# Performance work log

Measured on AMD Instinct MI355X. Metric: run time of the kernel, lower is better.

Reference implementation:

```python
import jax, jax.numpy as jnp
import numpy as np

H = 32; W = 32; C = 128; K = 3
FS = K * K                      # filter_size = 9
CH = H - K + 1; CW = W - K + 1
F = CH * CW                     # num_convs = 900
HW = H * W                      # 1024
TEMP = 1.0                      # softmax_temp
EPS = 1e-5                      # masked_softmax epsilon
B = 8


def _build_masks():
    # local_indices[f] = flat indices of the K x K window f (row-major),
    # matching compute_input_mask with stride=1, no stochastic stride.
    idx = np.zeros((F, FS), dtype=np.int32)
    f = 0
    for i in range(CH):
        for j in range(CW):
            rows = np.arange(i, i + K)[:, None]
            cols = np.arange(j, j + K)[None, :]
            idx[f] = (rows * W + cols).reshape(-1)
            f += 1
    # global mask = (1 - local_mask) * (1 - padding_mask); padding_mask == 0 for 'valid'
    gmask = np.ones((F, HW), dtype=np.float32)
    gmask[np.arange(F)[:, None], idx] = 0.0
    return jnp.asarray(idx), jnp.asarray(gmask)


def setup_inputs() -> dict:
    key = jax.random.key(0)
    ks = jax.random.split(key, 8)
    bound = 1.0 / np.sqrt(C)  # torch nn.Linear default init
    u = lambda k, shape: jax.random.uniform(k, shape, jnp.float32, -bound, bound)
    batch = jax.random.normal(ks[0], (B, H, W, C), jnp.float32)
    Wq = u(ks[1], (C, C)); bq = u(ks[2], (C,))
    Wk = u(ks[3], (C, C)); bk = u(ks[4], (C,))
    wv = u(ks[5], (C, 1)); bv = u(ks[6], (1,))
    local_indices, gmask = _build_masks()
    return {"batch": batch, "Wq": Wq, "bq": bq, "Wk": Wk, "bk": bk,
            "wv": wv, "bv": bv, "gmask": gmask, "local_indices": local_indices}


def reference(batch, Wq, bq, Wk, bk, wv, bv, gmask, local_indices):
    # Approach '4': per-window local queries attend over global (non-window)
    # pixels; scalar values gate the local patch pixels; gated patch sums to
    # one output pixel per window. Valid padding => local pixels are unmasked
    # and the masked softmax zeroes out window/padding positions, so the
    # per-window masked linear transforms reduce exactly to full-image
    # transforms gathered/masked afterwards (no [F,B,H,W,C] materialization).
    b = batch.shape[0]
    xf = batch.reshape(b, HW, C)
    Q = xf @ Wq.T + bq                         # [B,HW,C] query_transform
    Kf = xf @ Wk.T + bk                        # [B,HW,C] key_transform
    V = (xf @ wv + bv)[..., 0]                 # [B,HW]   value_transform (C->1)
    Qg = Q[:, local_indices]                   # [B,F,FS,C] local queries (gather)
    Xl = xf[:, local_indices]                  # [B,F,FS,C] local patch features
    compat = jnp.einsum('bfpc,bqc->bfpq', Qg, Kf) / TEMP   # [B,F,FS,HW]
    # masked_softmax: exp * mask / (sum + eps), no max-subtraction (faithful)
    exps = jnp.exp(compat) * gmask[None, :, None, :]
    attn = exps / (exps.sum(-1, keepdims=True) + EPS)
    gates = jnp.einsum('bfpq,bq->bfp', attn, V)            # [B,F,FS] scalar gates
    out = jnp.einsum('bfp,bfpc->bfc', gates, Xl)           # [B,F,C]
    return out.reshape(b, CH, CW, C)
```

## Files before the change

### kernel.cpp

```cpp
#include <hip/hip_runtime.h>

#define BATCH 8
#define HW_N  1024
#define CD    128
#define W_IMG 32
#define CH_O  30
#define F_N   900

#define OFF_Q16 0u
#define OFF_K16 2097152u
#define OFF_V   4194304u
#define OFF_D   4227072u
#define OFF_TP  5046272u
#define OFF_TVP 5570560u
#define OFF_WQF 6094848u
#define OFF_WKF 6127616u

typedef _Float16 f16x8 __attribute__((ext_vector_type(8)));
typedef _Float16 f16x4 __attribute__((ext_vector_type(4)));
typedef float    f32x4 __attribute__((ext_vector_type(4)));

__device__ __forceinline__ size_t frag_off(int R, int k) {
    return (size_t)(R >> 4) * 2048 +
           (size_t)((((k >> 5) * 4 + ((k >> 3) & 3)) * 128) + ((R & 15) * 8) + (k & 7));
}

__device__ __forceinline__ void async16(const void* g, void* l) {
    __builtin_amdgcn_global_load_lds(
        (const __attribute__((address_space(1))) unsigned int*)g,
        (__attribute__((address_space(3))) unsigned int*)l,
        16, 0, 0);
}

__global__ __launch_bounds__(256) void prep_kernel(
    const float* __restrict__ Wq, const float* __restrict__ Wk,
    _Float16* __restrict__ WqF, _Float16* __restrict__ WkF)
{
    int id = blockIdx.x * 256 + threadIdx.x;
    int c  = id >> 4;
    int kc = id & 15;
    size_t src = (size_t)c * CD + kc * 8;
    size_t dst = frag_off(c, kc * 8);

    float vq[8], vk[8];
    *(float4*)&vq[0] = *(const float4*)&Wq[src];
    *(float4*)&vq[4] = *(const float4*)&Wq[src + 4];
    *(float4*)&vk[0] = *(const float4*)&Wk[src];
    *(float4*)&vk[4] = *(const float4*)&Wk[src + 4];

    f16x8 qh, kh;
#pragma unroll
    for (int e = 0; e < 8; ++e) {
        qh[e] = (_Float16)vq[e];
        kh[e] = (_Float16)vk[e];
    }
    *(f16x8*)&WqF[dst] = qh;
    *(f16x8*)&WkF[dst] = kh;
}

__global__ __launch_bounds__(256) void qkv_kernel(
    const float* __restrict__ xf,
    const float* __restrict__ bq, const float* __restrict__ bk,
    const float* __restrict__ wv, const float* __restrict__ bv,
    const _Float16* __restrict__ WqF, const _Float16* __restrict__ WkF,
    _Float16* __restrict__ Q16, _Float16* __restrict__ K16,
    float* __restrict__ V)
{
    __shared__ float    xs[16][132];
    __shared__ _Float16 xh[2048];

    const int t = threadIdx.x;
    const int rowbase = blockIdx.x * 16;

#pragma unroll
    for (int m = 0; m < 2; ++m) {
        int id = t + 256 * m;
        int r  = id >> 5;
        int c4 = id & 31;
        float4 v4 = *(const float4*)&xf[(size_t)(rowbase + r) * CD + c4 * 4];
        *(float4*)&xs[r][c4 * 4] = v4;
        int c = c4 * 4;
        int off = ((c >> 5) * 4 + ((c >> 3) & 3)) * 128 + r * 8 + (c & 7);
        f16x4 hh;
        hh[0] = (_Float16)v4.x; hh[1] = (_Float16)v4.y;
        hh[2] = (_Float16)v4.z; hh[3] = (_Float16)v4.w;
        *(f16x4*)&xh[off] = hh;
    }
    __syncthreads();

    const int w    = t >> 6;
    const int lane = t & 63;
    const int q    = lane >> 4;
    const int i    = lane & 15;

    f32x4 aq[2], ak[2];
#pragma unroll
    for (int ct = 0; ct < 2; ++ct) {
        aq[ct] = (f32x4){0.f, 0.f, 0.f, 0.f};
        ak[ct] = (f32x4){0.f, 0.f, 0.f, 0.f};
    }

#pragma unroll
    for (int ks = 0; ks < 4; ++ks) {
        const int aoff = (ks * 4 + q) * 128 + i * 8;
        f16x8 ah = *(f16x8*)&xh[aoff];
#pragma unroll
        for (int ct = 0; ct < 2; ++ct) {
            size_t boff = (size_t)(w * 2 + ct) * 2048 + (size_t)(ks * 4 + q) * 128 + i * 8;
            f16x8 bq8 = *(const f16x8*)&WqF[boff];
            f16x8 bk8 = *(const f16x8*)&WkF[boff];
            aq[ct] = __builtin_amdgcn_mfma_f32_16x16x32_f16(ah, bq8, aq[ct], 0, 0, 0);
            ak[ct] = __builtin_amdgcn_mfma_f32_16x16x32_f16(ah, bk8, ak[ct], 0, 0, 0);
        }
    }

#pragma unroll
    for (int ct = 0; ct < 2; ++ct) {
        int c = (w * 2 + ct) * 16 + i;
        float bqv = bq[c], bkv = bk[c];
#pragma unroll
        for (int g = 0; g < 4; ++g) {
            int R = rowbase + q * 4 + g;
            size_t o = frag_off(R, c);
            Q16[o] = (_Float16)(aq[ct][g] + bqv);
            K16[o] = (_Float16)(ak[ct][g] + bkv);
        }
    }

    if (t < 16) {
        float s = 0.f;
#pragma unroll 8
        for (int k = 0; k < CD; ++k) s += xs[t][k] * wv[k];
        V[rowbase + t] = s + bv[0];
    }
}

#define A_OFF 0
#define B_OFF 16384
#define VS_OFF 32768
#define SCR2 16896
#define ATTN_LDS_TOTAL 33792

__global__ __launch_bounds__(256) void attn_kernel(
    const _Float16* __restrict__ Q16, const _Float16* __restrict__ K16,
    const float* __restrict__ V,
    double* __restrict__ Tp, double* __restrict__ TVp,
    float* __restrict__ D)
{
    extern __shared__ char lds[];
    _Float16* Ah = (_Float16*)(lds + A_OFF);
    _Float16* Bh = (_Float16*)(lds + B_OFF);
    float*    Vs = (float*)(lds + VS_OFF);

    const int b  = blockIdx.x;
    const int rb = blockIdx.y;
    const int cb = blockIdx.z;
    const int t  = threadIdx.x;
    const int w    = t >> 6;
    const int lane = t & 63;
    const int q    = lane >> 4;
    const int i    = lane & 15;
    const int wy = w >> 1, wx = w & 1;

    if (t < 128) Vs[t] = V[b * HW_N + cb * 128 + t];

    f32x4 acc[4][4];
#pragma unroll
    for (int r = 0; r < 4; ++r)
#pragma unroll
        for (int f = 0; f < 4; ++f) acc[r][f] = (f32x4){0.f, 0.f, 0.f, 0.f};

    const size_t abase = (size_t)(b * 8 + rb) * 16384;
    const size_t bbase = (size_t)(b * 8 + cb) * 16384;

    for (int kh = 0; kh < 2; ++kh) {
        __syncthreads();
#pragma unroll
        for (int m = 0; m < 4; ++m) {
            int id = t + 256 * m;
            size_t goff = (size_t)(id >> 7) * 2048 + kh * 1024 + (id & 127) * 8;
            int loff = id * 8;
            async16(Q16 + abase + goff, Ah + loff);
            async16(K16 + bbase + goff, Bh + loff);
        }
        asm volatile("s_waitcnt vmcnt(0)" ::: "memory");
        __syncthreads();

#pragma unroll
        for (int kcl = 0; kcl < 2; ++kcl) {
            f16x8 a4[4], b4[4];
#pragma unroll
            for (int r = 0; r < 4; ++r) {
                int ao = (((wy * 4 + r) * 2 + kcl) * 4 + q) * 128 + i * 8;
                a4[r] = *(f16x8*)&Ah[ao];
                int bo = (((wx * 4 + r) * 2 + kcl) * 4 + q) * 128 + i * 8;
                b4[r] = *(f16x8*)&Bh[bo];
            }
#pragma unroll
            for (int r = 0; r < 4; ++r)
#pragma unroll
                for (int f = 0; f < 4; ++f)
                    acc[r][f] = __builtin_amdgcn_mfma_f32_16x16x32_f16(
                        a4[r], b4[f], acc[r][f], 0, 0, 0);
        }
    }

    float st[4][4], stv[4][4];
#pragma unroll
    for (int r = 0; r < 4; ++r)
#pragma unroll
        for (int g = 0; g < 4; ++g) { st[r][g] = 0.f; stv[r][g] = 0.f; }

    const bool band = (cb - rb <= 1) && (rb - cb <= 1);

#pragma unroll
    for (int f = 0; f < 4; ++f) {
        int col_local = wx * 64 + f * 16 + i;
        int hw_c = cb * 128 + col_local;
        float v = Vs[col_local];
        int cimg_r = hw_c >> 5, cimg_c = hw_c & 31;
#pragma unroll
        for (int r = 0; r < 4; ++r)
#pragma unroll
            for (int g = 0; g < 4; ++g) {
                float e = __expf(acc[r][f][g]);
                st[r][g]  += e;
                stv[r][g] += e * v;
                if (band) {
                    int row_local = wy * 64 + r * 16 + q * 4 + g;
                    int hw_r = rb * 128 + row_local;
                    int dy = cimg_r - (hw_r >> 5);
                    int dx = cimg_c - (hw_r & 31);
                    if ((unsigned)(dy + 2) <= 4u && (unsigned)(dx + 2) <= 4u)
                        D[(size_t)(b * HW_N + hw_r) * 25 + (dy + 2) * 5 + (dx + 2)] = e;
                }
            }
    }

    __syncthreads();
    float* scrT  = (float*)lds;
    float* scrTV = (float*)(lds + SCR2);
#pragma unroll
    for (int r = 0; r < 4; ++r)
#pragma unroll
        for (int g = 0; g < 4; ++g) {
            int rl = wy * 64 + r * 16 + q * 4 + g;
            scrT [rl * 33 + wx * 16 + i] = st[r][g];
            scrTV[rl * 33 + wx * 16 + i] = stv[r][g];
        }
    __syncthreads();
    if (t < 128) {
        double s = 0.0;
#pragma unroll
        for (int c = 0; c < 32; ++c) s += (double)scrT[t * 33 + c];
        Tp[(size_t)(b * HW_N + rb * 128 + t) * 8 + cb] = s;
    } else {
        int tt = t - 128;
        double s = 0.0;
#pragma unroll
        for (int c = 0; c < 32; ++c) s += (double)scrTV[tt * 33 + c];
        TVp[(size_t)(b * HW_N + rb * 128 + tt) * 8 + cb] = s;
    }
}

__global__ __launch_bounds__(256) void gate_out_kernel(
    const float* __restrict__ xf, const float* __restrict__ V,
    const double* __restrict__ Tp, const double* __restrict__ TVp,
    const float* __restrict__ D, float* __restrict__ out)
{
    const int fi = blockIdx.x;
    const int b  = blockIdx.y;
    const int t  = threadIdx.x;

    __shared__ float  xs[96 * 128];
    __shared__ float  gates[32][9];
    __shared__ double Ts[96], TVs[96];

#pragma unroll
    for (int m = 0; m < 12; ++m) {
        int id   = t + 256 * m;
        int srow = id >> 5;
        int c4   = id & 31;
        int r3   = srow >> 5, colc = srow & 31;
        *(float4*)&xs[srow * 128 + c4 * 4] =
            *(const float4*)&xf[((size_t)(b * 32 + fi + r3) * 32 + colc) * CD + c4 * 4];
    }

    if (t < 96) {
        int R = b * HW_N + (fi + (t >> 5)) * W_IMG + (t & 31);
        double s = 0.0;
#pragma unroll
        for (int c = 0; c < 8; ++c) s += Tp[(size_t)R * 8 + c];
        Ts[t] = s;
    } else if (t >= 128 && t < 224) {
        int tt = t - 128;
        int R = b * HW_N + (fi + (tt >> 5)) * W_IMG + (tt & 31);
        double s = 0.0;
#pragma unroll
        for (int c = 0; c < 8; ++c) s += TVp[(size_t)R * 8 + c];
        TVs[tt] = s;
    }
    __syncthreads();

    for (int g = t; g < 270; g += 256) {
        int fj = g / 9, p = g % 9;
        int pr = p / 3, pc = p % 3;
        int lrow = pr * 32 + fj + pc;
        int ip = (fi + pr) * W_IMG + (fj + pc);
        const float* Drow = &D[(size_t)(b * HW_N + ip) * 25];
        double se = 0.0, sev = 0.0;
#pragma unroll
        for (int qq = 0; qq < 9; ++qq) {
            int qr = qq / 3, qc = qq % 3;
            float e = Drow[(qr - pr + 2) * 5 + (qc - pc + 2)];
            se  += (double)e;
            sev += (double)(e * V[b * HW_N + (fi + qr) * W_IMG + (fj + qc)]);
        }
        double denom = Ts[lrow] - se + 1e-5;
        double numer = TVs[lrow] - sev;
        gates[fj][p] = (float)(numer / denom);
    }
    __syncthreads();

    const int c4  = t & 31;
    const int fjl = t >> 5;
#pragma unroll
    for (int it = 0; it < 4; ++it) {
        int fj = fjl + 8 * it;
        if (fj < CH_O) {
            f32x4 o = (f32x4){0.f, 0.f, 0.f, 0.f};
#pragma unroll
            for (int p = 0; p < 9; ++p) {
                int pr = p / 3, pc = p % 3;
                f32x4 x = *(f32x4*)&xs[(pr * 32 + fj + pc) * 128 + c4 * 4];
                float gv = gates[fj][p];
                o += gv * x;
            }
            *(f32x4*)&out[((size_t)(b * F_N) + fi * CH_O + fj) * CD + c4 * 4] = o;
        }
    }
}

extern "C" void kernel_launch(void* const* d_in, const int* in_sizes, int n_in,
                              void* d_out, int out_size, void* d_ws, size_t ws_size,
                              hipStream_t stream)
{
    (void)in_sizes; (void)n_in; (void)out_size; (void)ws_size;
    const float* batch = (const float*)d_in[0];
    const float* Wq    = (const float*)d_in[1];
    const float* bq    = (const float*)d_in[2];
    const float* Wk    = (const float*)d_in[3];
    const float* bk    = (const float*)d_in[4];
    const float* wv    = (const float*)d_in[5];
    const float* bv    = (const float*)d_in[6];

    char*      ws  = (char*)d_ws;
    _Float16*  Q16 = (_Float16*)(ws + OFF_Q16);
    _Float16*  K16 = (_Float16*)(ws + OFF_K16);
    float*     V   = (float*)(ws + OFF_V);
    float*     D   = (float*)(ws + OFF_D);
    double*    Tp  = (double*)(ws + OFF_TP);
    double*    TVp = (double*)(ws + OFF_TVP);
    _Float16*  WqF = (_Float16*)(ws + OFF_WQF);
    _Float16*  WkF = (_Float16*)(ws + OFF_WKF);
    float*     out = (float*)d_out;

    prep_kernel<<<dim3(8), dim3(256), 0, stream>>>(Wq, Wk, WqF, WkF);
    qkv_kernel<<<dim3(512), dim3(256), 0, stream>>>(batch, bq, bk, wv, bv,
                                                    WqF, WkF, Q16, K16, V);
    attn_kernel<<<dim3(8, 8, 8), dim3(256), ATTN_LDS_TOTAL, stream>>>(
        Q16, K16, V, Tp, TVp, D);
    gate_out_kernel<<<dim3(CH_O, BATCH), dim3(256), 0, stream>>>(batch, V, Tp, TVp, D, out);
}
```

Baseline: 96.78 us.

## Fuse weight conversion into QKV, stage outputs via LDS, single-shot attn load, split gate kernel

Drops the separate weight-prep kernel: each QKV block now loads fp32 Wq/Wk from global and converts them to fp16 fragments in registers. Q/K tiles are staged through LDS so the global stores become coalesced 16-byte writes, and the V dot product is spread over 128 threads with a shuffle reduction. The attention kernel loads the full K=128 Q and K tiles into 64KB of LDS in one pass instead of two halves, which removes a barrier round but raises LDS use per block and may lower occupancy. The gate/output kernel is split over two channel halves to double the grid and halve its LDS footprint, at the cost of recomputing the gates in both halves.

```diff
diff --git a/kernel.cpp b/kernel.cpp
--- a/kernel.cpp
+++ b/kernel.cpp
@@ -13,17 +13,10 @@
 #define OFF_D   4227072u
 #define OFF_TP  5046272u
 #define OFF_TVP 5570560u
-#define OFF_WQF 6094848u
-#define OFF_WKF 6127616u
 
 typedef _Float16 f16x8 __attribute__((ext_vector_type(8)));
 typedef _Float16 f16x4 __attribute__((ext_vector_type(4)));
 typedef float    f32x4 __attribute__((ext_vector_type(4)));
-
-__device__ __forceinline__ size_t frag_off(int R, int k) {
-    return (size_t)(R >> 4) * 2048 +
-           (size_t)((((k >> 5) * 4 + ((k >> 3) & 3)) * 128) + ((R & 15) * 8) + (k & 7));
-}
 
 __device__ __forceinline__ void async16(const void* g, void* l) {
     __builtin_amdgcn_global_load_lds(
@@ -32,45 +25,47 @@
         16, 0, 0);
 }
 
-__global__ __launch_bounds__(256) void prep_kernel(
-    const float* __restrict__ Wq, const float* __restrict__ Wk,
-    _Float16* __restrict__ WqF, _Float16* __restrict__ WkF)
-{
-    int id = blockIdx.x * 256 + threadIdx.x;
-    int c  = id >> 4;
-    int kc = id & 15;
-    size_t src = (size_t)c * CD + kc * 8;
-    size_t dst = frag_off(c, kc * 8);
-
-    float vq[8], vk[8];
-    *(float4*)&vq[0] = *(const float4*)&Wq[src];
-    *(float4*)&vq[4] = *(const float4*)&Wq[src + 4];
-    *(float4*)&vk[0] = *(const float4*)&Wk[src];
-    *(float4*)&vk[4] = *(const float4*)&Wk[src + 4];
-
-    f16x8 qh, kh;
-#pragma unroll
-    for (int e = 0; e < 8; ++e) {
-        qh[e] = (_Float16)vq[e];
-        kh[e] = (_Float16)vk[e];
-    }
-    *(f16x8*)&WqF[dst] = qh;
-    *(f16x8*)&WkF[dst] = kh;
+__device__ __forceinline__ f16x8 cvt8(const float* __restrict__ p) {
+    float4 a = *(const float4*)p;
+    float4 b = *(const float4*)(p + 4);
+    f16x8 h;
+    h[0] = (_Float16)a.x; h[1] = (_Float16)a.y;
+    h[2] = (_Float16)a.z; h[3] = (_Float16)a.w;
+    h[4] = (_Float16)b.x; h[5] = (_Float16)b.y;
+    h[6] = (_Float16)b.z; h[7] = (_Float16)b.w;
+    return h;
 }
 
 __global__ __launch_bounds__(256) void qkv_kernel(
     const float* __restrict__ xf,
+    const float* __restrict__ Wq, const float* __restrict__ Wk,
     const float* __restrict__ bq, const float* __restrict__ bk,
     const float* __restrict__ wv, const float* __restrict__ bv,
-    const _Float16* __restrict__ WqF, const _Float16* __restrict__ WkF,
     _Float16* __restrict__ Q16, _Float16* __restrict__ K16,
     float* __restrict__ V)
 {
     __shared__ float    xs[16][132];
     __shared__ _Float16 xh[2048];
+    __shared__ _Float16 qtile[2048];
+    __shared__ _Float16 ktile[2048];
 
     const int t = threadIdx.x;
     const int rowbase = blockIdx.x * 16;
+    const int w    = t >> 6;
+    const int lane = t & 63;
+    const int q    = lane >> 4;
+    const int i    = lane & 15;
+
+    f16x8 wqf[2][4], wkf[2][4];
+#pragma unroll
+    for (int ct = 0; ct < 2; ++ct) {
+        const size_t c = (size_t)((w * 2 + ct) * 16 + i);
+#pragma unroll
+        for (int ks = 0; ks < 4; ++ks) {
+            wqf[ct][ks] = cvt8(&Wq[c * CD + ks * 32 + q * 8]);
+            wkf[ct][ks] = cvt8(&Wk[c * CD + ks * 32 + q * 8]);
+        }
+    }
 
 #pragma unroll
     for (int m = 0; m < 2; ++m) {
@@ -88,11 +83,6 @@
     }
     __syncthreads();
 
-    const int w    = t >> 6;
-    const int lane = t & 63;
-    const int q    = lane >> 4;
-    const int i    = lane & 15;
-
     f32x4 aq[2], ak[2];
 #pragma unroll
     for (int ct = 0; ct < 2; ++ct) {
@@ -106,11 +96,8 @@
         f16x8 ah = *(f16x8*)&xh[aoff];
 #pragma unroll
         for (int ct = 0; ct < 2; ++ct) {
-            size_t boff = (size_t)(w * 2 + ct) * 2048 + (size_t)(ks * 4 + q) * 128 + i * 8;
-            f16x8 bq8 = *(const f16x8*)&WqF[boff];
-            f16x8 bk8 = *(const f16x8*)&WkF[boff];
-            aq[ct] = __builtin_amdgcn_mfma_f32_16x16x32_f16(ah, bq8, aq[ct], 0, 0, 0);
-            ak[ct] = __builtin_amdgcn_mfma_f32_16x16x32_f16(ah, bk8, ak[ct], 0, 0, 0);
+            aq[ct] = __builtin_amdgcn_mfma_f32_16x16x32_f16(ah, wqf[ct][ks], aq[ct], 0, 0, 0);
+            ak[ct] = __builtin_amdgcn_mfma_f32_16x16x32_f16(ah, wkf[ct][ks], ak[ct], 0, 0, 0);
         }
     }
 
@@ -118,28 +105,42 @@
     for (int ct = 0; ct < 2; ++ct) {
         int c = (w * 2 + ct) * 16 + i;
         float bqv = bq[c], bkv = bk[c];
+        int coff = ((c >> 5) * 4 + ((c >> 3) & 3)) * 128 + (c & 7);
 #pragma unroll
         for (int g = 0; g < 4; ++g) {
-            int R = rowbase + q * 4 + g;
-            size_t o = frag_off(R, c);
-            Q16[o] = (_Float16)(aq[ct][g] + bqv);
-            K16[o] = (_Float16)(ak[ct][g] + bkv);
-        }
-    }
-
-    if (t < 16) {
+            int off = coff + (q * 4 + g) * 8;
+            qtile[off] = (_Float16)(aq[ct][g] + bqv);
+            ktile[off] = (_Float16)(ak[ct][g] + bkv);
+        }
+    }
+    __syncthreads();
+
+    {
+        f16x8 qv = *(f16x8*)&qtile[t * 8];
+        f16x8 kv = *(f16x8*)&ktile[t * 8];
+        *(f16x8*)&Q16[(size_t)rowbase * 128 + t * 8] = qv;
+        *(f16x8*)&K16[(size_t)rowbase * 128 + t * 8] = kv;
+    }
+
+    if (t < 128) {
+        int r = t >> 3, l = t & 7;
         float s = 0.f;
-#pragma unroll 8
-        for (int k = 0; k < CD; ++k) s += xs[t][k] * wv[k];
-        V[rowbase + t] = s + bv[0];
+#pragma unroll
+        for (int k = 0; k < 16; ++k) {
+            int c = l + k * 8;
+            s += xs[r][c] * wv[c];
+        }
+        s += __shfl_xor(s, 1);
+        s += __shfl_xor(s, 2);
+        s += __shfl_xor(s, 4);
+        if (l == 0) V[rowbase + r] = s + bv[0];
     }
 }
 
 #define A_OFF 0
-#define B_OFF 16384
-#define VS_OFF 32768
+#define B_OFF 32768
 #define SCR2 16896
-#define ATTN_LDS_TOTAL 33792
+#define ATTN_LDS_TOTAL 65536
 
 __global__ __launch_bounds__(256) void attn_kernel(
     const _Float16* __restrict__ Q16, const _Float16* __restrict__ K16,
@@ -150,7 +151,7 @@
     extern __shared__ char lds[];
     _Float16* Ah = (_Float16*)(lds + A_OFF);
     _Float16* Bh = (_Float16*)(lds + B_OFF);
-    float*    Vs = (float*)(lds + VS_OFF);
+    __shared__ float Vs[128];
 
     const int b  = blockIdx.x;
     const int rb = blockIdx.y;
@@ -164,45 +165,40 @@
 
     if (t < 128) Vs[t] = V[b * HW_N + cb * 128 + t];
 
-    f32x4 acc[4][4];
-#pragma unroll
-    for (int r = 0; r < 4; ++r)
-#pragma unroll
-        for (int f = 0; f < 4; ++f) acc[r][f] = (f32x4){0.f, 0.f, 0.f, 0.f};
-
     const size_t abase = (size_t)(b * 8 + rb) * 16384;
     const size_t bbase = (size_t)(b * 8 + cb) * 16384;
 
-    for (int kh = 0; kh < 2; ++kh) {
-        __syncthreads();
-#pragma unroll
-        for (int m = 0; m < 4; ++m) {
-            int id = t + 256 * m;
-            size_t goff = (size_t)(id >> 7) * 2048 + kh * 1024 + (id & 127) * 8;
-            int loff = id * 8;
-            async16(Q16 + abase + goff, Ah + loff);
-            async16(K16 + bbase + goff, Bh + loff);
-        }
-        asm volatile("s_waitcnt vmcnt(0)" ::: "memory");
-        __syncthreads();
-
-#pragma unroll
-        for (int kcl = 0; kcl < 2; ++kcl) {
-            f16x8 a4[4], b4[4];
-#pragma unroll
-            for (int r = 0; r < 4; ++r) {
-                int ao = (((wy * 4 + r) * 2 + kcl) * 4 + q) * 128 + i * 8;
-                a4[r] = *(f16x8*)&Ah[ao];
-                int bo = (((wx * 4 + r) * 2 + kcl) * 4 + q) * 128 + i * 8;
-                b4[r] = *(f16x8*)&Bh[bo];
-            }
-#pragma unroll
-            for (int r = 0; r < 4; ++r)
-#pragma unroll
-                for (int f = 0; f < 4; ++f)
-                    acc[r][f] = __builtin_amdgcn_mfma_f32_16x16x32_f16(
-                        a4[r], b4[f], acc[r][f], 0, 0, 0);
-        }
+#pragma unroll
+    for (int m = 0; m < 8; ++m) {
+        int id = t + 256 * m;
+        async16(Q16 + abase + (size_t)id * 8, Ah + id * 8);
+        async16(K16 + bbase + (size_t)id * 8, Bh + id * 8);
+    }
+    asm volatile("s_waitcnt vmcnt(0)" ::: "memory");
+    __syncthreads();
+
+    f32x4 acc[4][4];
+#pragma unroll
+    for (int r = 0; r < 4; ++r)
+#pragma unroll
+        for (int f = 0; f < 4; ++f) acc[r][f] = (f32x4){0.f, 0.f, 0.f, 0.f};
+
+#pragma unroll
+    for (int kcl = 0; kcl < 4; ++kcl) {
+        f16x8 a4[4], b4[4];
+#pragma unroll
+        for (int r = 0; r < 4; ++r) {
+            int ao = (wy * 4 + r) * 2048 + (kcl * 4 + q) * 128 + i * 8;
+            a4[r] = *(f16x8*)&Ah[ao];
+            int bo = (wx * 4 + r) * 2048 + (kcl * 4 + q) * 128 + i * 8;
+            b4[r] = *(f16x8*)&Bh[bo];
+        }
+#pragma unroll
+        for (int r = 0; r < 4; ++r)
+#pragma unroll
+            for (int f = 0; f < 4; ++f)
+                acc[r][f] = __builtin_amdgcn_mfma_f32_16x16x32_f16(
+                    a4[r], b4[f], acc[r][f], 0, 0, 0);
     }
 
     float st[4][4], stv[4][4];
@@ -270,20 +266,21 @@
 {
     const int fi = blockIdx.x;
     const int b  = blockIdx.y;
+    const int zh = blockIdx.z;
     const int t  = threadIdx.x;
 
-    __shared__ float  xs[96 * 128];
+    __shared__ float  xs[96 * 68];
     __shared__ float  gates[32][9];
     __shared__ double Ts[96], TVs[96];
 
 #pragma unroll
-    for (int m = 0; m < 12; ++m) {
+    for (int m = 0; m < 6; ++m) {
         int id   = t + 256 * m;
-        int srow = id >> 5;
-        int c4   = id & 31;
+        int srow = id >> 4;
+        int c4   = id & 15;
         int r3   = srow >> 5, colc = srow & 31;
-        *(float4*)&xs[srow * 128 + c4 * 4] =
-            *(const float4*)&xf[((size_t)(b * 32 + fi + r3) * 32 + colc) * CD + c4 * 4];
+        *(float4*)&xs[srow * 68 + c4 * 4] =
+            *(const float4*)&xf[((size_t)(b * 32 + fi + r3) * 32 + colc) * CD + zh * 64 + c4 * 4];
     }
 
     if (t < 96) {
@@ -322,21 +319,21 @@
     }
     __syncthreads();
 
-    const int c4  = t & 31;
-    const int fjl = t >> 5;
-#pragma unroll
-    for (int it = 0; it < 4; ++it) {
-        int fj = fjl + 8 * it;
+    const int c4  = t & 15;
+    const int fjl = t >> 4;
+#pragma unroll
+    for (int it = 0; it < 2; ++it) {
+        int fj = fjl + 16 * it;
         if (fj < CH_O) {
             f32x4 o = (f32x4){0.f, 0.f, 0.f, 0.f};
 #pragma unroll
             for (int p = 0; p < 9; ++p) {
                 int pr = p / 3, pc = p % 3;
-                f32x4 x = *(f32x4*)&xs[(pr * 32 + fj + pc) * 128 + c4 * 4];
+                f32x4 x = *(f32x4*)&xs[(pr * 32 + fj + pc) * 68 + c4 * 4];
                 float gv = gates[fj][p];
                 o += gv * x;
             }
-            *(f32x4*)&out[((size_t)(b * F_N) + fi * CH_O + fj) * CD + c4 * 4] = o;
+            *(f32x4*)&out[((size_t)(b * F_N) + fi * CH_O + fj) * CD + zh * 64 + c4 * 4] = o;
         }
     }
 }
@@ -361,14 +358,11 @@
     float*     D   = (float*)(ws + OFF_D);
     double*    Tp  = (double*)(ws + OFF_TP);
     double*    TVp = (double*)(ws + OFF_TVP);
-    _Float16*  WqF = (_Float16*)(ws + OFF_WQF);
-    _Float16*  WkF = (_Float16*)(ws + OFF_WKF);
     float*     out = (float*)d_out;
 
-    prep_kernel<<<dim3(8), dim3(256), 0, stream>>>(Wq, Wk, WqF, WkF);
-    qkv_kernel<<<dim3(512), dim3(256), 0, stream>>>(batch, bq, bk, wv, bv,
-                                                    WqF, WkF, Q16, K16, V);
+    qkv_kernel<<<dim3(512), dim3(256), 0, stream>>>(batch, Wq, Wk, bq, bk, wv, bv,
+                                                    Q16, K16, V);
     attn_kernel<<<dim3(8, 8, 8), dim3(256), ATTN_LDS_TOTAL, stream>>>(
         Q16, K16, V, Tp, TVp, D);
-    gate_out_kernel<<<dim3(CH_O, BATCH), dim3(256), 0, stream>>>(batch, V, Tp, TVp, D, out);
-}
+    gate_out_kernel<<<dim3(CH_O, BATCH, 2), dim3(256), 0, stream>>>(batch, V, Tp, TVp, D, out);
+}
```

New measurement: 97.96 us. About the same (+1.2%).
